# Kernel tuning notes

Measured on AMD Instinct MI355X. Metric: run time of the kernel, lower is better.

## Reference

```python
import jax, jax.numpy as jnp
import numpy as np

B, S, DM, H = 4, 1024, 1024, 16
DK = DM // H  # 64, must equal embeddim=64

def _linear(x, W, b):
    # torch nn.Linear: y = x @ W.T + b, W is [out, in]
    return jnp.matmul(x, W.T) + b

def setup_inputs() -> dict:
    key = jax.random.key(0)
    ks = jax.random.split(key, 40)
    inp = {}
    inp["query"] = jax.random.normal(ks[0], (B, S, DM), jnp.float32)
    inp["key"] = jax.random.normal(ks[1], (B, S, DM), jnp.float32)
    inp["value"] = jax.random.normal(ks[2], (B, S, DM), jnp.float32)
    inp["mask"] = jnp.ones((B, S, S), jnp.int32)
    def mk(i, dout, din):
        W = jax.random.normal(ks[i], (dout, din), jnp.float32) / np.sqrt(din).astype(np.float32)
        b = jax.random.normal(ks[i + 20], (dout,), jnp.float32) * 0.01
        return W, b
    # the 4 d_model x d_model projection linears (q, k, v, out)
    inp["Wq"], inp["bq"] = mk(3, DM, DM)
    inp["Wk"], inp["bk"] = mk(4, DM, DM)
    inp["Wv"], inp["bv"] = mk(5, DM, DM)
    inp["Wo"], inp["bo"] = mk(6, DM, DM)
    # the 64x64 refinement linears
    inp["Wkl"], inp["bkl"] = mk(7, DK, DK)   # key_linear
    inp["Wql"], inp["bql"] = mk(8, DK, DK)   # query_linear
    inp["Wq2"], inp["bq2"] = mk(9, DK, DK)   # query2_linear
    inp["Wvl"], inp["bvl"] = mk(10, DK, DK)  # value_linear
    inp["Wel"], inp["bel"] = mk(11, DK, DK)  # embed_linear
    return inp

def reference(query, key, value, mask,
              Wq, bq, Wk, bk, Wv, bv, Wo, bo,
              Wkl, bkl, Wql, bql, Wq2, bq2, Wvl, bvl, Wel, bel):
    b, s, dm = query.shape
    # project and split heads: [b, h, s, d_k]
    def split(x):
        return x.reshape(b, s, H, DK).transpose(0, 2, 1, 3)
    q = split(_linear(query, Wq, bq))
    k = split(_linear(key, Wk, bk))
    v = split(_linear(value, Wv, bv))
    # per-head 64x64 refinements with relu
    key_refine = jax.nn.relu(_linear(k, Wkl, bkl))
    q1 = jax.nn.relu(_linear(q, Wql, bql))
    q1 = jax.nn.relu(_linear(q1, Wel, bel))
    q2 = jax.nn.relu(_linear(q, Wq2, bq2))
    v_refine = jax.nn.relu(_linear(v, Wvl, bvl))
    # two attention-like matmuls (no 1/sqrt(d_k) scaling in original)
    qv = jnp.einsum("bhqd,bhkd->bhqk", q2, v_refine)
    kq = jnp.einsum("bhqd,bhkd->bhqk", q1, key_refine)
    m = mask[:, None, :, :]  # mask.unsqueeze(1)
    kq = jnp.where(m == 0, jnp.float32(-1e9), kq)
    attn = jax.nn.softmax(kq, axis=-1)
    # elementwise combine, then matmul against raw projected key (not value!)
    out = jnp.einsum("bhqk,bhkd->bhqd", attn * qv, k)
    out = out.transpose(0, 2, 1, 3).reshape(b, s, dm)
    return _linear(out, Wo, bo)
```

## Files before the change

kernel.cpp:

```cpp
#include <hip/hip_runtime.h>
#include <hip/hip_bf16.h>

#define B_  4
#define S_  1024
#define DM_ 1024
#define H_  16
#define DK_ 64

typedef unsigned short u16;
typedef __attribute__((ext_vector_type(8))) short bf16x8;
typedef __attribute__((ext_vector_type(4))) float f32x4;

__device__ __forceinline__ float bf2f(u16 u) {
    union { unsigned int i; float f; } c;
    c.i = ((unsigned int)u) << 16;
    return c.f;
}
__device__ __forceinline__ u16 f2bf(float f) {
    union { float f; unsigned int i; } c;
    c.f = f;
    unsigned int x = c.i;
    unsigned int lsb = (x >> 16) & 1u;
    x += 0x7fffu + lsb;
    return (u16)(x >> 16);
}
__device__ __forceinline__ u16 f2bf_fast(float f) {
    __hip_bfloat16 h = __float2bfloat16(f);
    return *reinterpret_cast<u16*>(&h);
}

__device__ __forceinline__ void async_ld16(const u16* g, u16* l) {
    __builtin_amdgcn_global_load_lds(
        (const __attribute__((address_space(1))) unsigned int*)(const void*)g,
        (__attribute__((address_space(3))) unsigned int*)(void*)l, 16, 0, 0);
}

__global__ void detect_kernel(const u16* __restrict__ q, int* __restrict__ flag) {
    int lane = threadIdx.x & 63;
    int cnt = 0;
#pragma unroll
    for (int i = 0; i < 4; ++i) {
        u16 u = q[2 * (lane * 4 + i)];
        int e = (u >> 7) & 0xFF;
        cnt += (e >= 100 && e <= 140) ? 1 : 0;
    }
#pragma unroll
    for (int off = 1; off < 64; off <<= 1) cnt += __shfl_xor(cnt, off, 64);
    if (lane == 0) *flag = (cnt < 128) ? 1 : 0;
}

#define NSEG 12
struct CvtArgs {
    const void* src[NSEG];
    void*       dst[NSEG];
    unsigned    off[NSEG + 1];
};

__global__ __launch_bounds__(256) void prep_kernel(
    CvtArgs a, unsigned total, const int* __restrict__ flag,
    const int* __restrict__ mask, int* __restrict__ tflags)
{
    const int tid = threadIdx.x;
    if (blockIdx.x < 512) {
        const int bx = blockIdx.x;
        const int kt = bx & 15, b = (bx >> 4) & 3, z = bx >> 6;
        int ok = 1;
#pragma unroll
        for (int i = tid; i < 128 * 16; i += 256) {
            int row = z * 128 + (i >> 4), seg = i & 15;
            int4 m = *(const int4*)&mask[((size_t)b * S_ + row) * S_ + kt * 64 + seg * 4];
            ok &= (m.x != 0) & (m.y != 0) & (m.z != 0) & (m.w != 0);
        }
        if (!ok) atomicOr(&tflags[b * 16 + kt], 1);
        return;
    }
    if (!*flag) return;
    unsigned v = (blockIdx.x - 512) * 256 + tid;
    if (v >= total) return;
    int s = 0;
    while (s < NSEG - 1 && v >= a.off[s + 1]) ++s;
    unsigned local = v - a.off[s];
    u16* dp = (u16*)a.dst[s] + (size_t)local * 8;
    const float* sp = (const float*)a.src[s] + (size_t)local * 8;
    float4 x = *(const float4*)sp, y = *(const float4*)(sp + 4);
    u16 t[8] = {f2bf(x.x), f2bf(x.y), f2bf(x.z), f2bf(x.w),
                f2bf(y.x), f2bf(y.y), f2bf(y.z), f2bf(y.w)};
    *(uint4*)dp = *(uint4*)t;
}

__global__ __launch_bounds__(256) void transpose_kernel(
    const u16* __restrict__ kp, u16* __restrict__ kpt)
{
    __shared__ u16 T[64][65];
    const int s0 = blockIdx.x * 64, h = blockIdx.y, b = blockIdx.z;
    const int tid = threadIdx.x;
    const size_t base = (size_t)b * S_ * DM_ + (size_t)h * DK_;
    for (int c = tid; c < 512; c += 256) {
        int row = c >> 3, cc = (c & 7) * 8;
        union { uint4 v; u16 u[8]; } x;
        x.v = *(const uint4*)&kp[base + (size_t)(s0 + row) * DM_ + cc];
#pragma unroll
        for (int j = 0; j < 8; ++j) T[row][cc + j] = x.u[j];
    }
    __syncthreads();
    const size_t baseT = (size_t)(b * H_ + h) * DK_ * S_;
    for (int c = tid; c < 512; c += 256) {
        int d = c >> 3, ss = (c & 7) * 8;
        u16 t[8];
#pragma unroll
        for (int j = 0; j < 8; ++j) t[j] = T[ss + j][d];
        *(uint4*)&kpt[baseT + (size_t)d * S_ + s0 + ss] = *(uint4*)t;
    }
}

struct QKVArgs {
    const u16* A0[3]; const u16* A1[3];
    const u16* W0[3]; const u16* W1[3];
    const void* bias[3];
    const u16* R10[3]; const u16* R11[3];
    const void* rb1[3];
    const u16* R20; const u16* R21; const void* rb2;
    const u16* R30; const u16* R31; const void* rb3;
    u16 *Kp, *q1b, *q2r, *krb, *vrb;
};

__global__ __launch_bounds__(256, 3) void qkv_fused_kernel(
    QKVArgs a, const int* __restrict__ flag)
{
    __shared__ __align__(16) u16 smem[16384];
    u16 (*As)[64] = (u16(*)[64])smem;
    u16 (*Ws)[64] = (u16(*)[64])(smem + 8192);

    const int z = blockIdx.z;
    const int f = *flag;
    const u16* __restrict__ A = f ? a.A1[z] : a.A0[z];
    const u16* __restrict__ W = f ? a.W1[z] : a.W0[z];
    const void* biasp = a.bias[z];

    const int m0   = blockIdx.y * 128;
    const int n0   = blockIdx.x * 128;
    const int tid  = threadIdx.x;
    const int w    = tid >> 6;
    const int lane = tid & 63;
    const int l16  = lane & 15;
    const int quad = lane >> 4;
    const int wr   = (w >> 1) * 64;
    const int wc   = (w & 1) * 64;

    const int srow = lane >> 3;
    const int sgrp = (lane & 7) ^ srow;

    f32x4 acc[4][4];
#pragma unroll
    for (int rt = 0; rt < 4; ++rt)
#pragma unroll
        for (int ct = 0; ct < 4; ++ct) acc[rt][ct] = (f32x4){0.f, 0.f, 0.f, 0.f};

    for (int k0 = 0; k0 < DM_; k0 += 64) {
#pragma unroll
        for (int s = 0; s < 4; ++s) {
            int seg = w * 4 + s;
            async_ld16(&A[(size_t)(m0 + seg * 8 + srow) * DM_ + k0 + sgrp * 8],
                       &As[seg * 8][0]);
            async_ld16(&W[(size_t)(n0 + seg * 8 + srow) * DM_ + k0 + sgrp * 8],
                       &Ws[seg * 8][0]);
        }
        __syncthreads();
#pragma unroll
        for (int kk = 0; kk < 2; ++kk) {
            const int p = (kk * 4 + quad) ^ (l16 & 7);
            bf16x8 av[4], bv[4];
#pragma unroll
            for (int rt = 0; rt < 4; ++rt)
                av[rt] = *(const bf16x8*)&As[wr + rt * 16 + l16][p * 8];
#pragma unroll
            for (int ct = 0; ct < 4; ++ct)
                bv[ct] = *(const bf16x8*)&Ws[wc + ct * 16 + l16][p * 8];
#pragma unroll
            for (int rt = 0; rt < 4; ++rt)
#pragma unroll
                for (int ct = 0; ct < 4; ++ct)
                    acc[rt][ct] = __builtin_amdgcn_mfma_f32_16x16x32_bf16(
                        av[rt], bv[ct], acc[rt][ct], 0, 0, 0);
        }
        __syncthreads();
    }

    const int hcol = n0 + wc;
    u16 (*Es)[64] = (u16(*)[64])(smem + w * 4096);

#pragma unroll
    for (int ct = 0; ct < 4; ++ct) {
        int col = hcol + ct * 16 + l16;
        float bv = f ? ((const float*)biasp)[col] : bf2f(((const u16*)biasp)[col]);
#pragma unroll
        for (int rt = 0; rt < 4; ++rt)
#pragma unroll
            for (int r = 0; r < 4; ++r) {
                int ml = rt * 16 + quad * 4 + r;
                int cl = ct * 16 + l16;
                u16 bb = f2bf(acc[rt][ct][r] + bv);
                if (z == 1) a.Kp[(size_t)(m0 + wr + ml) * DM_ + col] = bb;
                Es[ml][((((cl >> 3) ^ (ml & 7)) << 3) | (cl & 7))] = bb;
            }
    }

    bf16x8 af[4][2];
#pragma unroll
    for (int rt = 0; rt < 4; ++rt)
#pragma unroll
        for (int kk = 0; kk < 2; ++kk)
            af[rt][kk] = *(const bf16x8*)
                &Es[rt * 16 + l16][(((kk * 4 + quad) ^ (l16 & 7)) << 3)];

    const u16* R1 = f ? a.R11[z] : a.R10[z];
    bf16x8 wb[2][4];
#pragma unroll
    for (int kk = 0; kk < 2; ++kk)
#pragma unroll
        for (int ct = 0; ct < 4; ++ct)
            wb[kk][ct] = *(const bf16x8*)
                &R1[(size_t)(ct * 16 + l16) * 64 + kk * 32 + quad * 8];

    f32x4 r1[4][4];
#pragma unroll
    for (int rt = 0; rt < 4; ++rt)
#pragma unroll
        for (int ct = 0; ct < 4; ++ct) r1[rt][ct] = (f32x4){0.f, 0.f, 0.f, 0.f};
#pragma unroll
    for (int kk = 0; kk < 2; ++kk)
#pragma unroll
        for (int rt = 0; rt < 4; ++rt)
#pragma unroll
            for (int ct = 0; ct < 4; ++ct)
                r1[rt][ct] = __builtin_amdgcn_mfma_f32_16x16x32_bf16(
                    af[rt][kk], wb[kk][ct], r1[rt][ct], 0, 0, 0);

    if (z != 0) {
        const void* rb = a.rb1[z];
        u16* out = (z == 1) ? a.krb : a.vrb;
#pragma unroll
        for (int ct = 0; ct < 4; ++ct) {
            int cl = ct * 16 + l16;
            float bv = f ? ((const float*)rb)[cl] : bf2f(((const u16*)rb)[cl]);
#pragma unroll
            for (int rt = 0; rt < 4; ++rt)
#pragma unroll
                for (int r = 0; r < 4; ++r) {
                    float v = r1[rt][ct][r] + bv;
                    v = v > 0.f ? v : 0.f;
                    out[(size_t)(m0 + wr + rt * 16 + quad * 4 + r) * DM_ + hcol + cl]
                        = f2bf(v);
                }
        }
    } else {
        {
            const void* rb = a.rb1[0];
#pragma unroll
            for (int ct = 0; ct < 4; ++ct) {
                int cl = ct * 16 + l16;
                float bv = f ? ((const float*)rb)[cl] : bf2f(((const u16*)rb)[cl]);
#pragma unroll
                for (int rt = 0; rt < 4; ++rt)
#pragma unroll
                    for (int r = 0; r < 4; ++r) {
                        float v = r1[rt][ct][r] + bv;
                        v = v > 0.f ? v : 0.f;
                        int ml = rt * 16 + quad * 4 + r;
                        Es[ml][((((cl >> 3) ^ (ml & 7)) << 3) | (cl & 7))] = f2bf(v);
                    }
            }
        }
        {
            const u16* R3 = f ? a.R31 : a.R30;
#pragma unroll
            for (int kk = 0; kk < 2; ++kk)
#pragma unroll
                for (int ct = 0; ct < 4; ++ct)
                    wb[kk][ct] = *(const bf16x8*)
                        &R3[(size_t)(ct * 16 + l16) * 64 + kk * 32 + quad * 8];
            f32x4 r3[4][4];
#pragma unroll
            for (int rt = 0; rt < 4; ++rt)
#pragma unroll
                for (int ct = 0; ct < 4; ++ct) r3[rt][ct] = (f32x4){0.f, 0.f, 0.f, 0.f};
#pragma unroll
            for (int kk = 0; kk < 2; ++kk)
#pragma unroll
                for (int rt = 0; rt < 4; ++rt)
#pragma unroll
                    for (int ct = 0; ct < 4; ++ct)
                        r3[rt][ct] = __builtin_amdgcn_mfma_f32_16x16x32_bf16(
                            af[rt][kk], wb[kk][ct], r3[rt][ct], 0, 0, 0);
            const void* rb = a.rb3;
#pragma unroll
            for (int ct = 0; ct < 4; ++ct) {
                int cl = ct * 16 + l16;
                float bv = f ? ((const float*)rb)[cl] : bf2f(((const u16*)rb)[cl]);
#pragma unroll
                for (int rt = 0; rt < 4; ++rt)
#pragma unroll
                    for (int r = 0; r < 4; ++r) {
                        float v = r3[rt][ct][r] + bv;
                        v = v > 0.f ? v : 0.f;
                        a.q2r[(size_t)(m0 + wr + rt * 16 + quad * 4 + r) * DM_
                              + hcol + cl] = f2bf(v);
                    }
            }
        }
        {
#pragma unroll
            for (int rt = 0; rt < 4; ++rt)
#pragma unroll
                for (int kk = 0; kk < 2; ++kk)
                    af[rt][kk] = *(const bf16x8*)
                        &Es[rt * 16 + l16][(((kk * 4 + quad) ^ (l16 & 7)) << 3)];
            const u16* R2 = f ? a.R21 : a.R20;
#pragma unroll
            for (int kk = 0; kk < 2; ++kk)
#pragma unroll
                for (int ct = 0; ct < 4; ++ct)
                    wb[kk][ct] = *(const bf16x8*)
                        &R2[(size_t)(ct * 16 + l16) * 64 + kk * 32 + quad * 8];
            f32x4 r2[4][4];
#pragma unroll
            for (int rt = 0; rt < 4; ++rt)
#pragma unroll
                for (int ct = 0; ct < 4; ++ct) r2[rt][ct] = (f32x4){0.f, 0.f, 0.f, 0.f};
#pragma unroll
            for (int kk = 0; kk < 2; ++kk)
#pragma unroll
                for (int rt = 0; rt < 4; ++rt)
#pragma unroll
                    for (int ct = 0; ct < 4; ++ct)
                        r2[rt][ct] = __builtin_amdgcn_mfma_f32_16x16x32_bf16(
                            af[rt][kk], wb[kk][ct], r2[rt][ct], 0, 0, 0);
            const void* rb = a.rb2;
#pragma unroll
            for (int ct = 0; ct < 4; ++ct) {
                int cl = ct * 16 + l16;
                float bv = f ? ((const float*)rb)[cl] : bf2f(((const u16*)rb)[cl]);
#pragma unroll
                for (int rt = 0; rt < 4; ++rt)
#pragma unroll
                    for (int r = 0; r < 4; ++r) {
                        float v = r2[rt][ct][r] + bv;
                        v = v > 0.f ? v : 0.f;
                        a.q1b[(size_t)(m0 + wr + rt * 16 + quad * 4 + r) * DM_
                              + hcol + cl] = f2bf(v);
                    }
            }
        }
    }
}

__global__ __launch_bounds__(256, 3) void gemm_async_kernel(
    const u16* __restrict__ Ain, const u16* __restrict__ W0,
    const u16* __restrict__ W1, const void* __restrict__ biasp,
    void* __restrict__ Cp, const int* __restrict__ flag)
{
    __shared__ __align__(16) u16 As[128][64];
    __shared__ __align__(16) u16 Ws[128][64];

    const int f = *flag;
    const u16* __restrict__ W = f ? W1 : W0;

    const int m0   = blockIdx.y * 128;
    const int n0   = blockIdx.x * 128;
    const int tid  = threadIdx.x;
    const int w    = tid >> 6;
    const int lane = tid & 63;
    const int l16  = lane & 15;
    const int quad = lane >> 4;
    const int wr   = (w >> 1) * 64;
    const int wc   = (w & 1) * 64;

    const int srow = lane >> 3;
    const int sgrp = (lane & 7) ^ srow;

    f32x4 acc[4][4];
#pragma unroll
    for (int rt = 0; rt < 4; ++rt)
#pragma unroll
        for (int ct = 0; ct < 4; ++ct) acc[rt][ct] = (f32x4){0.f, 0.f, 0.f, 0.f};

    for (int k0 = 0; k0 < DM_; k0 += 64) {
#pragma unroll
        for (int s = 0; s < 4; ++s) {
            int seg = w * 4 + s;
            async_ld16(&Ain[(size_t)(m0 + seg * 8 + srow) * DM_ + k0 + sgrp * 8],
                       &As[seg * 8][0]);
            async_ld16(&W[(size_t)(n0 + seg * 8 + srow) * DM_ + k0 + sgrp * 8],
                       &Ws[seg * 8][0]);
        }
        __syncthreads();
#pragma unroll
        for (int kk = 0; kk < 2; ++kk) {
            const int p = (kk * 4 + quad) ^ (l16 & 7);
            bf16x8 av[4], bv[4];
#pragma unroll
            for (int rt = 0; rt < 4; ++rt)
                av[rt] = *(const bf16x8*)&As[wr + rt * 16 + l16][p * 8];
#pragma unroll
            for (int ct = 0; ct < 4; ++ct)
                bv[ct] = *(const bf16x8*)&Ws[wc + ct * 16 + l16][p * 8];
#pragma unroll
            for (int rt = 0; rt < 4; ++rt)
#pragma unroll
                for (int ct = 0; ct < 4; ++ct)
                    acc[rt][ct] = __builtin_amdgcn_mfma_f32_16x16x32_bf16(
                        av[rt], bv[ct], acc[rt][ct], 0, 0, 0);
        }
        __syncthreads();
    }

#pragma unroll
    for (int ct = 0; ct < 4; ++ct) {
        int col = n0 + wc + ct * 16 + l16;
        float bv = f ? ((const float*)biasp)[col] : bf2f(((const u16*)biasp)[col]);
#pragma unroll
        for (int rt = 0; rt < 4; ++rt)
#pragma unroll
            for (int r = 0; r < 4; ++r) {
                int row = m0 + wr + rt * 16 + quad * 4 + r;
                float v = acc[rt][ct][r] + bv;
                size_t idx = (size_t)row * DM_ + col;
                if (f) ((float*)Cp)[idx] = v;
                else   ((u16*)Cp)[idx]   = f2bf(v);
            }
    }
}

__global__ __launch_bounds__(256, 2) void attn_kernel(
    const u16* __restrict__ q1, const u16* __restrict__ q2,
    const u16* __restrict__ kr, const u16* __restrict__ vr,
    const u16* __restrict__ kpt, const int* __restrict__ mask,
    const int* __restrict__ tflags, u16* __restrict__ om)
{
    __shared__ __align__(16) u16 pts[4][32][72];

    const int bid  = blockIdx.x;
    const int orig = (bid & 7) * 64 + (bid >> 3);
    const int qt = orig & 7;
    const int h  = (orig >> 3) & 15;
    const int b  = orig >> 7;

    const int q0   = qt * 128;
    const int tid  = threadIdx.x;
    const int w    = tid >> 6;
    const int lane = tid & 63;
    const int l16  = lane & 15;
    const int quad = lane >> 4;

    const size_t base  = (size_t)b * S_ * DM_ + (size_t)h * DK_;
    const size_t baseT = (size_t)(b * H_ + h) * DK_ * S_;

    const u16* __restrict__ krL = kr  + base  + (size_t)l16 * DM_ + quad * 8;
    const u16* __restrict__ vrL = vr  + base  + (size_t)l16 * DM_ + quad * 8;
    const u16* __restrict__ ktL = kpt + baseT + (size_t)l16 * S_  + quad * 8;

    bf16x8 a1[2][2], a2[2][2];
#pragma unroll
    for (int rt = 0; rt < 2; ++rt) {
        const int qrow = q0 + w * 32 + rt * 16 + l16;
#pragma unroll
        for (int kk = 0; kk < 2; ++kk) {
            a1[rt][kk] = *(const bf16x8*)&q1[base + (size_t)qrow * DM_ + kk * 32 + quad * 8];
            a2[rt][kk] = *(const bf16x8*)&q2[base + (size_t)qrow * DM_ + kk * 32 + quad * 8];
        }
    }

    float m_run[2][4], l_run[2][4];
    f32x4 oacc[2][4];
#pragma unroll
    for (int rt = 0; rt < 2; ++rt)
#pragma unroll
        for (int r = 0; r < 4; ++r) { m_run[rt][r] = -1e30f; l_run[rt][r] = 0.f; }
#pragma unroll
    for (int rt = 0; rt < 2; ++rt)
#pragma unroll
        for (int ct = 0; ct < 4; ++ct) oacc[rt][ct] = (f32x4){0.f, 0.f, 0.f, 0.f};

    for (int kt = 0; kt < S_ / 64; ++kt) {
        const int k0 = kt * 64;
        const int tf = tflags[b * 16 + kt];

        f32x4 s1[2][4], s2[2][4];
#pragma unroll
        for (int rt = 0; rt < 2; ++rt)
#pragma unroll
            for (int ct = 0; ct < 4; ++ct) {
                s1[rt][ct] = (f32x4){0.f, 0.f, 0.f, 0.f};
                s2[rt][ct] = (f32x4){0.f, 0.f, 0.f, 0.f};
            }
        __builtin_amdgcn_s_setprio(1);
#pragma unroll
        for (int kk = 0; kk < 2; ++kk) {
            bf16x8 b1[4], b2[4];
#pragma unroll
            for (int ct = 0; ct < 4; ++ct) {
                b1[ct] = *(const bf16x8*)&krL[(size_t)(k0 + ct * 16) * DM_ + kk * 32];
                b2[ct] = *(const bf16x8*)&vrL[(size_t)(k0 + ct * 16) * DM_ + kk * 32];
            }
#pragma unroll
            for (int rt = 0; rt < 2; ++rt)
#pragma unroll
                for (int ct = 0; ct < 4; ++ct) {
                    s1[rt][ct] = __builtin_amdgcn_mfma_f32_16x16x32_bf16(
                        a1[rt][kk], b1[ct], s1[rt][ct], 0, 0, 0);
                    s2[rt][ct] = __builtin_amdgcn_mfma_f32_16x16x32_bf16(
                        a2[rt][kk], b2[ct], s2[rt][ct], 0, 0, 0);
                }
        }
        __builtin_amdgcn_s_setprio(0);

        if (tf) {
#pragma unroll
            for (int rt = 0; rt < 2; ++rt)
#pragma unroll
                for (int ct = 0; ct < 4; ++ct)
#pragma unroll
                    for (int r = 0; r < 4; ++r) {
                        int qrow = q0 + w * 32 + rt * 16 + quad * 4 + r;
                        int kc   = k0 + ct * 16 + l16;
                        if (mask[((size_t)b * S_ + qrow) * S_ + kc] == 0)
                            s1[rt][ct][r] = -1e9f;
                    }
        }

        float tmax[2][4];
#pragma unroll
        for (int rt = 0; rt < 2; ++rt)
#pragma unroll
            for (int r = 0; r < 4; ++r) tmax[rt][r] = -1e30f;
#pragma unroll
        for (int rt = 0; rt < 2; ++rt)
#pragma unroll
            for (int ct = 0; ct < 4; ++ct)
#pragma unroll
                for (int r = 0; r < 4; ++r)
                    tmax[rt][r] = fmaxf(tmax[rt][r], s1[rt][ct][r]);
#pragma unroll
        for (int off = 1; off < 16; off <<= 1)
#pragma unroll
            for (int rt = 0; rt < 2; ++rt)
#pragma unroll
                for (int r = 0; r < 4; ++r)
                    tmax[rt][r] = fmaxf(tmax[rt][r], __shfl_xor(tmax[rt][r], off, 64));

        float alpha[2][4], newm[2][4];
#pragma unroll
        for (int rt = 0; rt < 2; ++rt)
#pragma unroll
            for (int r = 0; r < 4; ++r) {
                newm[rt][r]  = fmaxf(m_run[rt][r], tmax[rt][r]);
                alpha[rt][r] = __expf(m_run[rt][r] - newm[rt][r]);
                m_run[rt][r] = newm[rt][r];
            }

        float psum[2][4] = {};
#pragma unroll
        for (int rt = 0; rt < 2; ++rt)
#pragma unroll
            for (int ct = 0; ct < 4; ++ct)
#pragma unroll
                for (int r = 0; r < 4; ++r) {
                    float p = __expf(s1[rt][ct][r] - newm[rt][r]);
                    psum[rt][r] += p;
                    pts[w][rt * 16 + quad * 4 + r][ct * 16 + l16] =
                        f2bf_fast(p * s2[rt][ct][r]);
                }
#pragma unroll
        for (int off = 1; off < 16; off <<= 1)
#pragma unroll
            for (int rt = 0; rt < 2; ++rt)
#pragma unroll
                for (int r = 0; r < 4; ++r)
                    psum[rt][r] += __shfl_xor(psum[rt][r], off, 64);
#pragma unroll
        for (int rt = 0; rt < 2; ++rt)
#pragma unroll
            for (int r = 0; r < 4; ++r)
                l_run[rt][r] = l_run[rt][r] * alpha[rt][r] + psum[rt][r];
#pragma unroll
        for (int rt = 0; rt < 2; ++rt)
#pragma unroll
            for (int ct = 0; ct < 4; ++ct)
#pragma unroll
                for (int r = 0; r < 4; ++r) oacc[rt][ct][r] *= alpha[rt][r];

        {
            __builtin_amdgcn_s_setprio(1);
            bf16x8 bb[2][4];
#pragma unroll
            for (int kk = 0; kk < 2; ++kk)
#pragma unroll
                for (int ct = 0; ct < 4; ++ct)
                    bb[kk][ct] = *(const bf16x8*)&ktL[(size_t)(ct * 16) * S_ + k0 + kk * 32];
#pragma unroll
            for (int rt = 0; rt < 2; ++rt)
#pragma unroll
                for (int kk = 0; kk < 2; ++kk) {
                    bf16x8 a = *(const bf16x8*)&pts[w][rt * 16 + l16][kk * 32 + quad * 8];
#pragma unroll
                    for (int ct = 0; ct < 4; ++ct)
                        oacc[rt][ct] = __builtin_amdgcn_mfma_f32_16x16x32_bf16(
                            a, bb[kk][ct], oacc[rt][ct], 0, 0, 0);
                }
            __builtin_amdgcn_s_setprio(0);
        }
    }

#pragma unroll
    for (int rt = 0; rt < 2; ++rt)
#pragma unroll
        for (int ct = 0; ct < 4; ++ct)
#pragma unroll
            for (int r = 0; r < 4; ++r) {
                int row = q0 + w * 32 + rt * 16 + quad * 4 + r;
                int col = ct * 16 + l16;
                float v = oacc[rt][ct][r] / l_run[rt][r];
                om[base + (size_t)row * DM_ + col] = f2bf_fast(v);
            }
}

extern "C" void kernel_launch(void* const* d_in, const int* in_sizes, int n_in,
                              void* d_out, int out_size, void* d_ws, size_t ws_size,
                              hipStream_t stream)
{
    const void* query = d_in[0];
    const void* key   = d_in[1];
    const void* value = d_in[2];
    const int*  mask  = (const int*)d_in[3];
    const void* Wq  = d_in[4];  const void* bq  = d_in[5];
    const void* Wk  = d_in[6];  const void* bk  = d_in[7];
    const void* Wv  = d_in[8];  const void* bv  = d_in[9];
    const void* Wo  = d_in[10]; const void* bo  = d_in[11];
    const void* Wkl = d_in[12]; const void* bkl = d_in[13];
    const void* Wql = d_in[14]; const void* bql = d_in[15];
    const void* Wq2 = d_in[16]; const void* bq2 = d_in[17];
    const void* Wvl = d_in[18]; const void* bvl = d_in[19];
    const void* Wel = d_in[20]; const void* bel = d_in[21];

    int* flag   = (int*)d_ws;
    int* tflags = (int*)d_ws + 4;
    u16* ws     = (u16*)((char*)d_ws + 512);
    const size_t BUF = (size_t)(B_ * S_) * DM_;
    u16* Kp  = ws + 0 * BUF;
    u16* krb = ws + 1 * BUF;
    u16* q1b = ws + 2 * BUF;
    u16* q2r = ws + 3 * BUF;
    u16* vrb = ws + 4 * BUF;
    u16* Om  = ws + 5 * BUF;
    u16* KpT = ws + 6 * BUF;
    u16* Qc  = ws + 7 * BUF;
    u16* Kc  = ws + 8 * BUF;
    u16* Vc  = ws + 9 * BUF;
    u16* Wbig = ws + 10 * BUF;
    u16* Wqc = Wbig + 0 * (size_t)(DM_ * DM_);
    u16* Wkc = Wbig + 1 * (size_t)(DM_ * DM_);
    u16* Wvc = Wbig + 2 * (size_t)(DM_ * DM_);
    u16* Woc = Wbig + 3 * (size_t)(DM_ * DM_);
    u16* Wsm = Wbig + 4 * (size_t)(DM_ * DM_);
    u16* Wklc = Wsm + 0 * (DK_ * DK_);
    u16* Wqlc = Wsm + 1 * (DK_ * DK_);
    u16* Welc = Wsm + 2 * (DK_ * DK_);
    u16* Wq2c = Wsm + 3 * (DK_ * DK_);
    u16* Wvlc = Wsm + 4 * (DK_ * DK_);

    const int M = B_ * S_;
    dim3 blk(256);

    detect_kernel<<<1, 64, 0, stream>>>((const u16*)query, flag);

    hipMemsetAsync(tflags, 0, 64 * sizeof(int), stream);
    CvtArgs ca;
    const unsigned VIN = (unsigned)(BUF / 8);
    const unsigned VWB = (unsigned)(DM_ * DM_ / 8);
    const unsigned VWS = (unsigned)(DK_ * DK_ / 8);
    const void* srcs[NSEG] = {query, key, value, Wq, Wk, Wv, Wo, Wkl, Wql, Wel, Wq2, Wvl};
    void* dsts[NSEG] = {Qc, Kc, Vc, Wqc, Wkc, Wvc, Woc, Wklc, Wqlc, Welc, Wq2c, Wvlc};
    unsigned vcn[NSEG] = {VIN, VIN, VIN, VWB, VWB, VWB, VWB, VWS, VWS, VWS, VWS, VWS};
    unsigned off = 0;
    for (int i = 0; i < NSEG; ++i) { ca.src[i] = srcs[i]; ca.dst[i] = dsts[i]; ca.off[i] = off; off += vcn[i]; }
    ca.off[NSEG] = off;
    prep_kernel<<<dim3(512 + (off + 255) / 256), blk, 0, stream>>>(ca, off, flag, mask, tflags);

    QKVArgs qa = {};
    qa.A0[0] = (const u16*)query; qa.A1[0] = Qc;
    qa.A0[1] = (const u16*)key;   qa.A1[1] = Kc;
    qa.A0[2] = (const u16*)value; qa.A1[2] = Vc;
    qa.W0[0] = (const u16*)Wq; qa.W1[0] = Wqc;
    qa.W0[1] = (const u16*)Wk; qa.W1[1] = Wkc;
    qa.W0[2] = (const u16*)Wv; qa.W1[2] = Wvc;
    qa.bias[0] = bq; qa.bias[1] = bk; qa.bias[2] = bv;
    qa.R10[0] = (const u16*)Wql; qa.R11[0] = Wqlc; qa.rb1[0] = bql;
    qa.R10[1] = (const u16*)Wkl; qa.R11[1] = Wklc; qa.rb1[1] = bkl;
    qa.R10[2] = (const u16*)Wvl; qa.R11[2] = Wvlc; qa.rb1[2] = bvl;
    qa.R20 = (const u16*)Wel; qa.R21 = Welc; qa.rb2 = bel;
    qa.R30 = (const u16*)Wq2; qa.R31 = Wq2c; qa.rb3 = bq2;
    qa.Kp = Kp; qa.q1b = q1b; qa.q2r = q2r; qa.krb = krb; qa.vrb = vrb;
    dim3 gBig(DM_ / 128, M / 128, 3);
    qkv_fused_kernel<<<gBig, blk, 0, stream>>>(qa, flag);

    dim3 gT(S_ / 64, H_, B_);
    transpose_kernel<<<gT, blk, 0, stream>>>(Kp, KpT);

    attn_kernel<<<dim3(512), blk, 0, stream>>>(q1b, q2r, krb, vrb, KpT, mask, tflags, Om);

    dim3 gO(DM_ / 128, M / 128);
    gemm_async_kernel<<<gO, blk, 0, stream>>>(Om, (const u16*)Wo, Woc, bo, d_out, flag);
}
```

Baseline: 332.4 us.

## Stage K/V/K^T tiles in double-buffered LDS with async loads in attention

Each attention block now copies the key-refine, value-refine and transposed-key tiles into double-buffered shared memory with async global-to-LDS loads, using an XOR swizzle. The next tile is prefetched while the current one is being computed on. Previously all four waves loaded the same tiles from global memory separately, so this removes redundant global/L2 traffic and hides load latency. In exchange it uses more LDS, which may limit occupancy, and it adds a block-wide barrier on every iteration.

Measured after the change: 309.9 us. 1.07x faster.

```diff
diff --git a/kernel.cpp b/kernel.cpp
--- a/kernel.cpp
+++ b/kernel.cpp
@@ -437,6 +437,9 @@
     const u16* __restrict__ kpt, const int* __restrict__ mask,
     const int* __restrict__ tflags, u16* __restrict__ om)
 {
+    __shared__ __align__(16) u16 krs[2][64][64];
+    __shared__ __align__(16) u16 vrs[2][64][64];
+    __shared__ __align__(16) u16 kts[2][64][64];
     __shared__ __align__(16) u16 pts[4][32][72];
 
     const int bid  = blockIdx.x;
@@ -455,9 +458,27 @@
     const size_t base  = (size_t)b * S_ * DM_ + (size_t)h * DK_;
     const size_t baseT = (size_t)(b * H_ + h) * DK_ * S_;
 
-    const u16* __restrict__ krL = kr  + base  + (size_t)l16 * DM_ + quad * 8;
-    const u16* __restrict__ vrL = vr  + base  + (size_t)l16 * DM_ + quad * 8;
-    const u16* __restrict__ ktL = kpt + baseT + (size_t)l16 * S_  + quad * 8;
+    const int srow = lane >> 3;
+    const int sgrp = (lane & 7) ^ srow;
+
+#define STAGE_TILES(buf, kn)                                                   \
+    {                                                                          \
+        _Pragma("unroll")                                                      \
+        for (int i = 0; i < 6; ++i) {                                          \
+            int s_ = w * 6 + i;                                                \
+            int t_ = s_ >> 3;                                                  \
+            int r8 = (s_ & 7) * 8;                                             \
+            if (t_ == 0)                                                       \
+                async_ld16(&kr[base + (size_t)((kn) + r8 + srow) * DM_ +       \
+                               sgrp * 8], &krs[buf][r8][0]);                   \
+            else if (t_ == 1)                                                  \
+                async_ld16(&vr[base + (size_t)((kn) + r8 + srow) * DM_ +       \
+                               sgrp * 8], &vrs[buf][r8][0]);                   \
+            else                                                               \
+                async_ld16(&kpt[baseT + (size_t)(r8 + srow) * S_ + (kn) +      \
+                                sgrp * 8], &kts[buf][r8][0]);                  \
+        }                                                                      \
+    }
 
     bf16x8 a1[2][2], a2[2][2];
 #pragma unroll
@@ -481,8 +502,16 @@
 #pragma unroll
         for (int ct = 0; ct < 4; ++ct) oacc[rt][ct] = (f32x4){0.f, 0.f, 0.f, 0.f};
 
+    STAGE_TILES(0, 0)
+    __syncthreads();
+
     for (int kt = 0; kt < S_ / 64; ++kt) {
-        const int k0 = kt * 64;
+        const int cur = kt & 1;
+        const int k0  = kt * 64;
+        const bool pf = (kt + 1 < S_ / 64);
+
+        if (pf) STAGE_TILES(cur ^ 1, k0 + 64)
+
         const int tf = tflags[b * 16 + kt];
 
         f32x4 s1[2][4], s2[2][4];
@@ -496,11 +525,12 @@
         __builtin_amdgcn_s_setprio(1);
 #pragma unroll
         for (int kk = 0; kk < 2; ++kk) {
+            const int p = ((kk * 4 + quad) ^ (l16 & 7)) * 8;
             bf16x8 b1[4], b2[4];
 #pragma unroll
             for (int ct = 0; ct < 4; ++ct) {
-                b1[ct] = *(const bf16x8*)&krL[(size_t)(k0 + ct * 16) * DM_ + kk * 32];
-                b2[ct] = *(const bf16x8*)&vrL[(size_t)(k0 + ct * 16) * DM_ + kk * 32];
+                b1[ct] = *(const bf16x8*)&krs[cur][ct * 16 + l16][p];
+                b2[ct] = *(const bf16x8*)&vrs[cur][ct * 16 + l16][p];
             }
 #pragma unroll
             for (int rt = 0; rt < 2; ++rt)
@@ -593,10 +623,12 @@
             __builtin_amdgcn_s_setprio(1);
             bf16x8 bb[2][4];
 #pragma unroll
-            for (int kk = 0; kk < 2; ++kk)
+            for (int kk = 0; kk < 2; ++kk) {
+                const int p = ((kk * 4 + quad) ^ (l16 & 7)) * 8;
 #pragma unroll
                 for (int ct = 0; ct < 4; ++ct)
-                    bb[kk][ct] = *(const bf16x8*)&ktL[(size_t)(ct * 16) * S_ + k0 + kk * 32];
+                    bb[kk][ct] = *(const bf16x8*)&kts[cur][ct * 16 + l16][p];
+            }
 #pragma unroll
             for (int rt = 0; rt < 2; ++rt)
 #pragma unroll
@@ -609,6 +641,8 @@
                 }
             __builtin_amdgcn_s_setprio(0);
         }
+
+        if (pf) __syncthreads();
     }
 
 #pragma unroll
@@ -622,6 +656,7 @@
                 float v = oacc[rt][ct][r] / l_run[rt][r];
                 om[base + (size_t)row * DM_ + col] = f2bf_fast(v);
             }
+#undef STAGE_TILES
 }
 
 extern "C" void kernel_launch(void* const* d_in, const int* in_sizes, int n_in,
```
